# Performance work log

Measured on AMD Instinct MI355X. Metric: run time of the kernel, lower is better.

The kernel has to match this reference:

```python
import jax, jax.numpy as jnp
import numpy as np

T, N, D = 4096, 32768, 1024

def setup_inputs() -> dict:
    key = jax.random.key(0)
    k1, k2 = jax.random.split(key)
    x = jax.random.normal(k1, (T, D), dtype=jnp.float32)
    embeddings = jax.random.normal(k2, (N, D), dtype=jnp.float32)
    return {"x": x, "embeddings": embeddings}

def reference(x, embeddings):
    # scores: [T, N] = x @ E^T (unscaled single-head attention, Q=x, K=V=E)
    scores = jnp.einsum('td,nd->tn', x, embeddings)
    probs = jax.nn.softmax(scores, axis=-1)
    # out: [T, D] = probs @ E
    return jnp.einsum('tn,nd->td', probs, embeddings)
```

## Files before the change

kernel.cpp:

```cpp
#include <hip/hip_runtime.h>
#include <stdint.h>

#define T_DIM 4096
#define N_DIM 32768
#define D_DIM 1024
#define QB 64
#define KB 32
#define KSPLIT 4
#define ITERS (N_DIM / KSPLIT / KB)
#define NKB_TOT (N_DIM / KB)
#define NKEYS_PER (N_DIM / KSPLIT)
#define NBLOCKS ((T_DIM / QB) * KSPLIT)

typedef _Float16 f16;
typedef _Float16 f16x8 __attribute__((ext_vector_type(8)));
typedef _Float16 f16x4 __attribute__((ext_vector_type(4)));
typedef float f32x4 __attribute__((ext_vector_type(4)));

#define SWZ(q, k0) ((k0) ^ ((((q) >> 2) & 3) << 2))

struct __align__(16) Lds {
  f16   K[2][KB * D_DIM];
  float Spart[2][QB][40];
  f16   P[QB][40];
  float srow[QB];
  float linv[QB];
};

__global__ void e16_build(const float* __restrict__ E, f16* __restrict__ E16) {
  size_t i8 = (size_t)(blockIdx.x * 256 + threadIdx.x) * 8;
  float4 a = *(const float4*)(E + i8);
  float4 b = *(const float4*)(E + i8 + 4);
  f16x8 v = {(f16)a.x,(f16)a.y,(f16)a.z,(f16)a.w,
             (f16)b.x,(f16)b.y,(f16)b.z,(f16)b.w};
  *(f16x8*)(E16 + i8) = v;
}

__global__ void w2_build(const float* __restrict__ E, f16* __restrict__ W2) {
  int kb = blockIdx.x >> 2;
  int dg = blockIdx.x & 3;
  int d  = dg * 256 + threadIdx.x;
  for (int kq = 0; kq < 4; ++kq) {
    int k0 = kq * 8;
    f16x8 v;
    #pragma unroll
    for (int j = 0; j < 8; ++j)
      v[j] = (f16)E[(size_t)(kb*32 + k0 + j) * D_DIM + d];
    *(f16x8*)(W2 + (size_t)kb * (D_DIM*KB) + (size_t)d*KB + k0) = v;
  }
}

__device__ __forceinline__ void gl_lds16(const void* g, void* l) {
  auto* gp = reinterpret_cast<const __attribute__((address_space(1))) uint32_t*>(
      reinterpret_cast<uintptr_t>(g));
  auto* lp = reinterpret_cast<__attribute__((address_space(3))) uint32_t*>(
      reinterpret_cast<uintptr_t>(l));
  __builtin_amdgcn_global_load_lds(gp, lp, 16, 0, 0);
}

__global__ __launch_bounds__(512, 1)
void cboe_attn(const float* __restrict__ X, const f16* __restrict__ E16,
               const f16* __restrict__ W2, f16* __restrict__ O16,
               float* __restrict__ ML)
{
  extern __shared__ char smem_raw[];
  Lds& L = *reinterpret_cast<Lds*>(smem_raw);
  const int tid  = threadIdx.x;
  const int lane = tid & 63;
  const int w    = tid >> 6;
  const int c    = lane & 15;
  const int g    = lane >> 4;
  const int qt   = w >> 1;
  const int dh   = w & 1;
  const int wd   = w * 128;
  const int qtile = blockIdx.x & 63;
  const int ks    = blockIdx.x >> 6;
  const int qb    = qtile * QB;
  const size_t key0 = (size_t)ks * NKEYS_PER;
  const int sq    = tid >> 3;
  const int kslot = tid & 7;

  f16x8 qf[16];
  {
    const float* qrow = X + (size_t)(qb + qt*16 + c) * D_DIM + dh*512;
    #pragma unroll
    for (int kc = 0; kc < 16; ++kc) {
      float4 a = *(const float4*)(qrow + kc*32 + g*8);
      float4 b = *(const float4*)(qrow + kc*32 + g*8 + 4);
      qf[kc] = (f16x8){(f16)a.x,(f16)a.y,(f16)a.z,(f16)a.w,
                       (f16)b.x,(f16)b.y,(f16)b.z,(f16)b.w};
    }
  }

  f32x4 acc[4][8];
  #pragma unroll
  for (int q2 = 0; q2 < 4; ++q2)
    #pragma unroll
    for (int dt = 0; dt < 8; ++dt) acc[q2][dt] = (f32x4){0.f,0.f,0.f,0.f};

  float m_run = -1.0e30f, l_run = 0.0f;

  #define STAGE(IT) do {                                                      \
    const char* gt_ = (const char*)(E16 + (key0 + (size_t)(IT)*KB)*D_DIM);    \
    char* lb_ = (char*)&L.K[(IT) & 1][0];                                     \
    _Pragma("unroll")                                                         \
    for (int r_ = 0; r_ < 8; ++r_) {                                          \
      uint32_t a_ = (uint32_t)(w*8192 + r_*1024 + lane*16);                   \
      uint32_t s_ = a_ ^ (((a_ >> 11) & 7) << 4);                             \
      gl_lds16(gt_ + s_, lb_ + w*8192 + r_*1024);                             \
    }                                                                         \
  } while (0)

  STAGE(0);
  STAGE(1);

  const int sxor  = (c & 7) << 4;
  const int dbase = dh*1024 + g*16;

  for (int it = 0; it < ITERS; ++it) {
    const char* KLB = (const char*)&L.K[it & 1][0];

    asm volatile("s_waitcnt vmcnt(8)" ::: "memory");
    __builtin_amdgcn_s_barrier();
    asm volatile("" ::: "memory");

    #pragma unroll
    for (int kt = 0; kt < 2; ++kt) {
      const int keyb = (kt*16 + c) << 11;
      f32x4 sA = (f32x4){0.f,0.f,0.f,0.f};
      f32x4 sB = (f32x4){0.f,0.f,0.f,0.f};
      __builtin_amdgcn_s_setprio(1);
      #pragma unroll
      for (int kc = 0; kc < 8; ++kc) {
        f16x8 ak0 = *(const f16x8*)(KLB + keyb + ((dbase + kc*64) ^ sxor));
        f16x8 ak1 = *(const f16x8*)(KLB + keyb + ((dbase + (kc+8)*64) ^ sxor));
        sA = __builtin_amdgcn_mfma_f32_16x16x32_f16(ak0, qf[kc],   sA, 0, 0, 0);
        sB = __builtin_amdgcn_mfma_f32_16x16x32_f16(ak1, qf[kc+8], sB, 0, 0, 0);
      }
      __builtin_amdgcn_s_setprio(0);
      f32x4 s = sA + sB;
      const int q = qt*16 + c;
      *(f32x4*)&L.Spart[dh][q][SWZ(q, kt*16 + g*4)] = s;
    }

    asm volatile("s_waitcnt lgkmcnt(0)" ::: "memory");
    __builtin_amdgcn_s_barrier();
    asm volatile("" ::: "memory");

    const f16* vbase = W2 + (key0/KB + it) * (size_t)(D_DIM*KB);
    f16x8 bv[8];
    #pragma unroll
    for (int dt = 0; dt < 8; ++dt)
      bv[dt] = *(const f16x8*)(vbase + (size_t)(wd + dt*16 + c)*KB + g*8);
    if (it + 2 < ITERS) STAGE(it + 2);

    f32x4 sv = *(const f32x4*)&L.Spart[0][sq][SWZ(sq, kslot*4)];
    sv += *(const f32x4*)&L.Spart[1][sq][SWZ(sq, kslot*4)];
    float tm = fmaxf(fmaxf(sv[0],sv[1]), fmaxf(sv[2],sv[3]));
    tm = fmaxf(tm, __shfl_xor(tm, 1));
    tm = fmaxf(tm, __shfl_xor(tm, 2));
    tm = fmaxf(tm, __shfl_xor(tm, 4));
    const bool upd = tm > m_run + 8.0f;
    const float mn = upd ? tm : m_run;
    const float scale = upd ? __expf(m_run - mn) : 1.0f;
    float p0 = __expf(sv[0]-mn), p1 = __expf(sv[1]-mn);
    float p2 = __expf(sv[2]-mn), p3 = __expf(sv[3]-mn);
    *(f16x4*)&L.P[sq][kslot*4] = (f16x4){(f16)p0,(f16)p1,(f16)p2,(f16)p3};
    float ps = (p0+p1)+(p2+p3);
    ps += __shfl_xor(ps, 1);
    ps += __shfl_xor(ps, 2);
    ps += __shfl_xor(ps, 4);
    l_run = l_run * scale + ps;
    m_run = mn;
    if (kslot == 0) L.srow[sq] = scale;

    asm volatile("s_waitcnt lgkmcnt(0)" ::: "memory");
    __builtin_amdgcn_s_barrier();
    asm volatile("" ::: "memory");

    #pragma unroll
    for (int q2 = 0; q2 < 4; ++q2) {
      f32x4 sc = *(const f32x4*)&L.srow[q2*16 + g*4];
      bool need = (sc[0]!=1.f)|(sc[1]!=1.f)|(sc[2]!=1.f)|(sc[3]!=1.f);
      if (__any(need)) {
        #pragma unroll
        for (int dt = 0; dt < 8; ++dt) {
          acc[q2][dt][0]*=sc[0]; acc[q2][dt][1]*=sc[1];
          acc[q2][dt][2]*=sc[2]; acc[q2][dt][3]*=sc[3];
        }
      }
    }
    #pragma unroll
    for (int q2 = 0; q2 < 4; ++q2) {
      f16x8 ap = *(const f16x8*)&L.P[q2*16 + c][g*8];
      __builtin_amdgcn_s_setprio(1);
      #pragma unroll
      for (int dt = 0; dt < 8; ++dt)
        acc[q2][dt] = __builtin_amdgcn_mfma_f32_16x16x32_f16(ap, bv[dt], acc[q2][dt], 0, 0, 0);
      __builtin_amdgcn_s_setprio(0);
    }
  }
  #undef STAGE

  if (kslot == 0) {
    size_t qg = (size_t)qb + sq;
    ML[((size_t)ks * T_DIM + qg) * 2 + 0] = m_run;
    ML[((size_t)ks * T_DIM + qg) * 2 + 1] = l_run;
    L.linv[sq] = 1.0f / l_run;
  }
  __syncthreads();
  #pragma unroll
  for (int q2 = 0; q2 < 4; ++q2) {
    f32x4 li = *(const f32x4*)&L.linv[q2*16 + g*4];
    #pragma unroll
    for (int dt = 0; dt < 8; ++dt)
      #pragma unroll
      for (int r = 0; r < 4; ++r)
        O16[((size_t)ks * T_DIM + qb + q2*16 + 4*g + r) * D_DIM + wd + dt*16 + c] =
            (f16)(acc[q2][dt][r] * li[r]);
  }
}

__global__ void combine(const f16* __restrict__ O16, const float* __restrict__ ML,
                        float* __restrict__ Out) {
  int q  = blockIdx.x;
  int d0 = threadIdx.x * 4;
  float m[KSPLIT], l[KSPLIT];
  float M = -1.0e30f;
  #pragma unroll
  for (int ks = 0; ks < KSPLIT; ++ks) {
    m[ks] = ML[((size_t)ks * T_DIM + q) * 2 + 0];
    l[ks] = ML[((size_t)ks * T_DIM + q) * 2 + 1];
    M = fmaxf(M, m[ks]);
  }
  float W = 0.f, wk[KSPLIT];
  #pragma unroll
  for (int ks = 0; ks < KSPLIT; ++ks) {
    wk[ks] = l[ks] * __expf(m[ks] - M);
    W += wk[ks];
  }
  float inv = 1.0f / W;
  float o0 = 0.f, o1 = 0.f, o2 = 0.f, o3 = 0.f;
  #pragma unroll
  for (int ks = 0; ks < KSPLIT; ++ks) {
    f16x4 v = *(const f16x4*)(O16 + ((size_t)ks * T_DIM + q) * D_DIM + d0);
    o0 += wk[ks] * (float)v[0];
    o1 += wk[ks] * (float)v[1];
    o2 += wk[ks] * (float)v[2];
    o3 += wk[ks] * (float)v[3];
  }
  float4 o = {o0 * inv, o1 * inv, o2 * inv, o3 * inv};
  *(float4*)(Out + (size_t)q * D_DIM + d0) = o;
}

__global__ void cboe_naive(const float* __restrict__ X, const float* __restrict__ E,
                           float* __restrict__ Out) {
  int row  = blockIdx.x * 4 + (threadIdx.x >> 6);
  int lane = threadIdx.x & 63;
  float xq[16], acc[16];
  #pragma unroll
  for (int j = 0; j < 16; ++j) {
    xq[j] = X[(size_t)row * D_DIM + lane*16 + j];
    acc[j] = 0.f;
  }
  float m = -1.0e30f, l = 0.f;
  for (int key = 0; key < N_DIM; ++key) {
    const float* er = E + (size_t)key * D_DIM + lane*16;
    float ev[16];
    float s = 0.f;
    #pragma unroll
    for (int j = 0; j < 16; ++j) { ev[j] = er[j]; s += xq[j] * ev[j]; }
    #pragma unroll
    for (int sh = 1; sh < 64; sh <<= 1) s += __shfl_xor(s, sh);
    float mn = fmaxf(m, s);
    float sc = __expf(m - mn);
    float p  = __expf(s - mn);
    l = l * sc + p;
    #pragma unroll
    for (int j = 0; j < 16; ++j) acc[j] = acc[j] * sc + p * ev[j];
    m = mn;
  }
  #pragma unroll
  for (int j = 0; j < 16; ++j)
    Out[(size_t)row * D_DIM + lane*16 + j] = acc[j] / l;
}

extern "C" void kernel_launch(void* const* d_in, const int* in_sizes, int n_in,
                              void* d_out, int out_size, void* d_ws, size_t ws_size,
                              hipStream_t stream) {
  const float* X  = (const float*)d_in[0];
  const float* Eg = (const float*)d_in[1];
  float* Out = (float*)d_out;

  const size_t szE16 = (size_t)N_DIM * D_DIM * sizeof(f16);
  const size_t szW2  = (size_t)NKB_TOT * D_DIM * KB * sizeof(f16);
  const size_t szO16 = (size_t)KSPLIT * T_DIM * D_DIM * sizeof(f16);
  const size_t szML  = (size_t)KSPLIT * T_DIM * 2 * sizeof(float);
  const size_t need  = szE16 + szW2 + szO16 + szML;

  if (!d_ws || ws_size < need) {
    cboe_naive<<<dim3(T_DIM/4), dim3(256), 0, stream>>>(X, Eg, Out);
    return;
  }

  char* p = (char*)d_ws;
  f16*   E16 = (f16*)p;   p += szE16;
  f16*   W2  = (f16*)p;   p += szW2;
  f16*   O16 = (f16*)p;   p += szO16;
  float* ML  = (float*)p;

  e16_build<<<dim3((N_DIM * D_DIM) / (256 * 8)), dim3(256), 0, stream>>>(Eg, E16);
  w2_build<<<dim3(NKB_TOT * 4), dim3(256), 0, stream>>>(Eg, W2);

  const int shmem = (int)sizeof(Lds);
  hipFuncSetAttribute(reinterpret_cast<const void*>(&cboe_attn),
                      hipFuncAttributeMaxDynamicSharedMemorySize, shmem);
  cboe_attn<<<dim3(NBLOCKS), dim3(512), shmem, stream>>>(X, E16, W2, O16, ML);
  combine<<<dim3(T_DIM), dim3(256), 0, stream>>>(O16, ML, Out);
}
```

Baseline: 1.938 ms.

## Software-pipeline PV MFMA one iteration behind softmax to drop a barrier

Double-buffers the P and scale arrays in LDS so the P·V MFMA for iteration it-1 runs in the same phase as the softmax of iteration it. This removes one block-wide barrier per iteration and gives the V-fragment global loads a whole iteration to land before use. The vmcnt wait is raised to account for the extra in-flight loads, and an epilogue handles the last PV step. The cost is more LDS and register pressure from keeping bv live across the loop.

```diff
diff --git a/kernel.cpp b/kernel.cpp
--- a/kernel.cpp
+++ b/kernel.cpp
@@ -22,8 +22,8 @@
 struct __align__(16) Lds {
   f16   K[2][KB * D_DIM];
   float Spart[2][QB][40];
-  f16   P[QB][40];
-  float srow[QB];
+  f16   P[2][QB][40];
+  float srow[2][QB];
   float linv[QB];
 };
 
@@ -99,6 +99,7 @@
     for (int dt = 0; dt < 8; ++dt) acc[q2][dt] = (f32x4){0.f,0.f,0.f,0.f};
 
   float m_run = -1.0e30f, l_run = 0.0f;
+  f16x8 bv[8];
 
   #define STAGE(IT) do {                                                      \
     const char* gt_ = (const char*)(E16 + (key0 + (size_t)(IT)*KB)*D_DIM);    \
@@ -118,11 +119,12 @@
   const int dbase = dh*1024 + g*16;
 
   for (int it = 0; it < ITERS; ++it) {
-    const char* KLB = (const char*)&L.K[it & 1][0];
-
-    asm volatile("s_waitcnt vmcnt(8)" ::: "memory");
+    if (it == 0) asm volatile("s_waitcnt vmcnt(8) lgkmcnt(0)" ::: "memory");
+    else         asm volatile("s_waitcnt vmcnt(16) lgkmcnt(0)" ::: "memory");
     __builtin_amdgcn_s_barrier();
     asm volatile("" ::: "memory");
+
+    const char* KLB = (const char*)&L.K[it & 1][0];
 
     #pragma unroll
     for (int kt = 0; kt < 2; ++kt) {
@@ -147,40 +149,71 @@
     __builtin_amdgcn_s_barrier();
     asm volatile("" ::: "memory");
 
-    const f16* vbase = W2 + (key0/KB + it) * (size_t)(D_DIM*KB);
-    f16x8 bv[8];
-    #pragma unroll
-    for (int dt = 0; dt < 8; ++dt)
-      bv[dt] = *(const f16x8*)(vbase + (size_t)(wd + dt*16 + c)*KB + g*8);
+    {
+      f32x4 sv = *(const f32x4*)&L.Spart[0][sq][SWZ(sq, kslot*4)];
+      sv += *(const f32x4*)&L.Spart[1][sq][SWZ(sq, kslot*4)];
+      float tm = fmaxf(fmaxf(sv[0],sv[1]), fmaxf(sv[2],sv[3]));
+      tm = fmaxf(tm, __shfl_xor(tm, 1));
+      tm = fmaxf(tm, __shfl_xor(tm, 2));
+      tm = fmaxf(tm, __shfl_xor(tm, 4));
+      const bool upd = tm > m_run + 8.0f;
+      const float mn = upd ? tm : m_run;
+      const float scale = upd ? __expf(m_run - mn) : 1.0f;
+      float p0 = __expf(sv[0]-mn), p1 = __expf(sv[1]-mn);
+      float p2 = __expf(sv[2]-mn), p3 = __expf(sv[3]-mn);
+      *(f16x4*)&L.P[it & 1][sq][kslot*4] = (f16x4){(f16)p0,(f16)p1,(f16)p2,(f16)p3};
+      float ps = (p0+p1)+(p2+p3);
+      ps += __shfl_xor(ps, 1);
+      ps += __shfl_xor(ps, 2);
+      ps += __shfl_xor(ps, 4);
+      l_run = l_run * scale + ps;
+      m_run = mn;
+      if (kslot == 0) L.srow[it & 1][sq] = scale;
+    }
+
+    if (it > 0) {
+      const int pp = (it - 1) & 1;
+      #pragma unroll
+      for (int q2 = 0; q2 < 4; ++q2) {
+        f32x4 sc = *(const f32x4*)&L.srow[pp][q2*16 + g*4];
+        bool need = (sc[0]!=1.f)|(sc[1]!=1.f)|(sc[2]!=1.f)|(sc[3]!=1.f);
+        if (__any(need)) {
+          #pragma unroll
+          for (int dt = 0; dt < 8; ++dt) {
+            acc[q2][dt][0]*=sc[0]; acc[q2][dt][1]*=sc[1];
+            acc[q2][dt][2]*=sc[2]; acc[q2][dt][3]*=sc[3];
+          }
+        }
+      }
+      #pragma unroll
+      for (int q2 = 0; q2 < 4; ++q2) {
+        f16x8 ap = *(const f16x8*)&L.P[pp][q2*16 + c][g*8];
+        __builtin_amdgcn_s_setprio(1);
+        #pragma unroll
+        for (int dt = 0; dt < 8; ++dt)
+          acc[q2][dt] = __builtin_amdgcn_mfma_f32_16x16x32_f16(ap, bv[dt], acc[q2][dt], 0, 0, 0);
+        __builtin_amdgcn_s_setprio(0);
+      }
+    }
+
+    {
+      const f16* vbase = W2 + (key0/KB + it) * (size_t)(D_DIM*KB);
+      #pragma unroll
+      for (int dt = 0; dt < 8; ++dt)
+        bv[dt] = *(const f16x8*)(vbase + (size_t)(wd + dt*16 + c)*KB + g*8);
+    }
     if (it + 2 < ITERS) STAGE(it + 2);
-
-    f32x4 sv = *(const f32x4*)&L.Spart[0][sq][SWZ(sq, kslot*4)];
-    sv += *(const f32x4*)&L.Spart[1][sq][SWZ(sq, kslot*4)];
-    float tm = fmaxf(fmaxf(sv[0],sv[1]), fmaxf(sv[2],sv[3]));
-    tm = fmaxf(tm, __shfl_xor(tm, 1));
-    tm = fmaxf(tm, __shfl_xor(tm, 2));
-    tm = fmaxf(tm, __shfl_xor(tm, 4));
-    const bool upd = tm > m_run + 8.0f;
-    const float mn = upd ? tm : m_run;
-    const float scale = upd ? __expf(m_run - mn) : 1.0f;
-    float p0 = __expf(sv[0]-mn), p1 = __expf(sv[1]-mn);
-    float p2 = __expf(sv[2]-mn), p3 = __expf(sv[3]-mn);
-    *(f16x4*)&L.P[sq][kslot*4] = (f16x4){(f16)p0,(f16)p1,(f16)p2,(f16)p3};
-    float ps = (p0+p1)+(p2+p3);
-    ps += __shfl_xor(ps, 1);
-    ps += __shfl_xor(ps, 2);
-    ps += __shfl_xor(ps, 4);
-    l_run = l_run * scale + ps;
-    m_run = mn;
-    if (kslot == 0) L.srow[sq] = scale;
-
-    asm volatile("s_waitcnt lgkmcnt(0)" ::: "memory");
-    __builtin_amdgcn_s_barrier();
-    asm volatile("" ::: "memory");
-
+  }
+  #undef STAGE
+
+  asm volatile("s_waitcnt lgkmcnt(0)" ::: "memory");
+  __builtin_amdgcn_s_barrier();
+  asm volatile("" ::: "memory");
+  {
+    const int pp = (ITERS - 1) & 1;
     #pragma unroll
     for (int q2 = 0; q2 < 4; ++q2) {
-      f32x4 sc = *(const f32x4*)&L.srow[q2*16 + g*4];
+      f32x4 sc = *(const f32x4*)&L.srow[pp][q2*16 + g*4];
       bool need = (sc[0]!=1.f)|(sc[1]!=1.f)|(sc[2]!=1.f)|(sc[3]!=1.f);
       if (__any(need)) {
         #pragma unroll
@@ -192,15 +225,12 @@
     }
     #pragma unroll
     for (int q2 = 0; q2 < 4; ++q2) {
-      f16x8 ap = *(const f16x8*)&L.P[q2*16 + c][g*8];
-      __builtin_amdgcn_s_setprio(1);
+      f16x8 ap = *(const f16x8*)&L.P[pp][q2*16 + c][g*8];
       #pragma unroll
       for (int dt = 0; dt < 8; ++dt)
         acc[q2][dt] = __builtin_amdgcn_mfma_f32_16x16x32_f16(ap, bv[dt], acc[q2][dt], 0, 0, 0);
-      __builtin_amdgcn_s_setprio(0);
-    }
-  }
-  #undef STAGE
+    }
+  }
 
   if (kslot == 0) {
     size_t qg = (size_t)qb + sq;
```

After: 4.143 ms. 114% more time.
